# Optimization experiments

Hardware: AMD Instinct MI355X
Metric: run time of the kernel (lower is better)

## Reference

```python
import jax, jax.numpy as jnp
import numpy as np

N = 8192
IN_F = 512
OUT_F = 512
N_SUB = 8


def setup_inputs() -> dict:
    key = jax.random.key(0)
    k1, k2, k3, k4 = jax.random.split(key, 4)
    input_features = jax.random.normal(k1, (N, IN_F), dtype=jnp.float32)
    # dense adjacency with small positive entries (normalized-adj-like)
    adj = jax.random.uniform(k2, (N, N), dtype=jnp.float32) / N
    subspace_labels = jax.random.randint(k3, (N,), 0, N_SUB, dtype=jnp.int32)
    # kaiming-uniform-style init per subspace weight
    bound = float(np.sqrt(6.0 / IN_F))
    W = jax.random.uniform(k4, (N_SUB, IN_F, OUT_F), dtype=jnp.float32,
                           minval=-bound, maxval=bound)
    return {"input_features": input_features, "adj": adj,
            "subspace_labels": subspace_labels, "W": W}


def reference(input_features, adj, subspace_labels, W):
    # Original: for each subspace s,
    #   output[mask_s] = adj[mask_s][:, mask_s] @ (X[mask_s] @ W[s])
    # Equivalently: per-node support uses that node's subspace weight, and
    # adjacency is masked to same-subspace pairs.
    n_sub = W.shape[0]
    support = jnp.zeros((input_features.shape[0], W.shape[2]),
                        dtype=input_features.dtype)
    for s in range(n_sub):  # small fixed loop over subspaces
        sel = (subspace_labels == s)[:, None]
        support = support + jnp.where(sel, input_features @ W[s], 0.0)
    # mask adjacency to intra-subspace edges: [N, N]
    same = (subspace_labels[:, None] == subspace_labels[None, :])
    masked_adj = jnp.where(same, adj, 0.0)
    return masked_adj @ support
```

## Files before the change

kernel.cpp:

```cpp
#include <hip/hip_runtime.h>
#include <hip/hip_bf16.h>

#define NN   8192
#define FF   512
#define NS   8
#define CAP  1152
#define KKT  (NS * CAP)

typedef __bf16 bf16x8 __attribute__((ext_vector_type(8)));
typedef float  f32x4  __attribute__((ext_vector_type(4)));

__global__ void bucket_kernel(const int* __restrict__ labels,
                              int* __restrict__ permP,
                              int* __restrict__ kk_of) {
    __shared__ int off8[NS];
    int t = threadIdx.x;
    if (t < NS) off8[t] = 0;
    for (int i = t; i < KKT; i += 256) permP[i] = -1;
    __syncthreads();
    for (int i = t; i < NN; i += 256) {
        int s = labels[i];
        int p = atomicAdd(&off8[s], 1);
        if (p < CAP) {
            int pos = s * CAP + p;
            permP[pos] = i;
            kk_of[i] = pos;
        } else {
            kk_of[i] = -1;
        }
    }
}

__global__ void wt_kernel(const float* __restrict__ W, __bf16* __restrict__ WT) {
    __shared__ float tile[32][33];
    int s  = blockIdx.z;
    int n0 = blockIdx.x * 32, k0 = blockIdx.y * 32;
    int tx = threadIdx.x, ty = threadIdx.y;
    const float* Ws = W + (size_t)s * FF * FF;
    for (int r = 0; r < 4; ++r) {
        int k = k0 + ty + r * 8;
        tile[ty + r * 8][tx] = Ws[(size_t)k * FF + n0 + tx];
    }
    __syncthreads();
    __bf16* WTs = WT + (size_t)s * FF * FF;
    for (int r = 0; r < 4; ++r) {
        int n = n0 + ty + r * 8;
        WTs[(size_t)n * FF + k0 + tx] = (__bf16)tile[tx][ty + r * 8];
    }
}

__global__ __launch_bounds__(512) void support_kernel(
        const float* __restrict__ X, const __bf16* __restrict__ WT,
        const int* __restrict__ permP, __bf16* __restrict__ supT) {
    __shared__ __align__(16) __bf16 Alds[4][32][8];
    __shared__ __align__(16) __bf16 Blds[4][512][8];
    __shared__ int nodes[32];
    const int t = threadIdx.x, lane = t & 63, w = t >> 6;
    const int ii0 = blockIdx.x * 32;
    const int seg = ii0 / CAP;
    const int mh = w & 1, nq = w >> 1, l15 = lane & 15, q = lane >> 4;
    f32x4 acc[8] = {};
    if (t < 32) nodes[t] = permP[ii0 + t];
    __syncthreads();
    const __bf16* Wseg = WT + (size_t)seg * FF * FF;
    for (int k0 = 0; k0 < FF; k0 += 32) {
        #pragma unroll
        for (int pass = 0; pass < 4; ++pass) {
            int slot = pass * 512 + t;
            int c = slot & 3, n = slot >> 2;
            uint4 tmp = *(const uint4*)(Wseg + (size_t)n * FF + k0 + c * 8);
            *(uint4*)&Blds[c][n][0] = tmp;
        }
        if (t < 256) {
            int m = t >> 3, c = t & 7;
            int node = nodes[m];
            __align__(8) __bf16 v[4];
            if (node >= 0) {
                float4 xv = *(const float4*)(X + (size_t)node * FF + k0 + c * 4);
                v[0] = (__bf16)xv.x; v[1] = (__bf16)xv.y;
                v[2] = (__bf16)xv.z; v[3] = (__bf16)xv.w;
            } else {
                v[0] = v[1] = v[2] = v[3] = (__bf16)0.0f;
            }
            int kq = c >> 1, off = (c & 1) * 4;
            *(uint2*)&Alds[kq][m][off] = *(uint2*)v;
        }
        __syncthreads();
        bf16x8 af = *(bf16x8*)&Alds[q][mh * 16 + l15][0];
        int nbase = nq * 128 + l15;
        #pragma unroll
        for (int nt = 0; nt < 8; ++nt) {
            bf16x8 bfr = *(bf16x8*)&Blds[q][nbase + nt * 16][0];
            acc[nt] = __builtin_amdgcn_mfma_f32_16x16x32_bf16(af, bfr, acc[nt], 0, 0, 0);
        }
        __syncthreads();
    }
    int kkb = ii0 + mh * 16 + q * 4;
    #pragma unroll
    for (int nt = 0; nt < 8; ++nt) {
        int n = nq * 128 + nt * 16 + l15;
        __align__(8) __bf16 v[4];
        #pragma unroll
        for (int r = 0; r < 4; ++r) v[r] = (__bf16)acc[nt][r];
        *(uint2*)(supT + (size_t)n * KKT + kkb) = *(uint2*)v;
    }
}

__global__ __launch_bounds__(256) void compact_kernel(
        const float* __restrict__ adj, const int* __restrict__ permP,
        const int* __restrict__ kk_of, __bf16* __restrict__ adjc) {
    int ii = blockIdx.x;
    int node = permP[ii];
    if (node < 0) return;
    int base = (ii / CAP) * CAP;
    __bf16* dst = adjc + (size_t)ii * CAP;
    const float4* arow = (const float4*)(adj + (size_t)node * NN);
    const int4*  kkrow = (const int4*)kk_of;
    int t = threadIdx.x;
    #pragma unroll
    for (int p = 0; p < NN / (256 * 4); ++p) {
        int idx = p * 256 + t;
        float4 a = arow[idx];
        int4  kk = kkrow[idx];
        int j;
        j = kk.x - base; if ((unsigned)j < CAP) dst[j] = (__bf16)a.x;
        j = kk.y - base; if ((unsigned)j < CAP) dst[j] = (__bf16)a.y;
        j = kk.z - base; if ((unsigned)j < CAP) dst[j] = (__bf16)a.z;
        j = kk.w - base; if ((unsigned)j < CAP) dst[j] = (__bf16)a.w;
    }
}

__global__ __launch_bounds__(512) void gemm_kernel(
        const __bf16* __restrict__ adjc, const __bf16* __restrict__ supT,
        const int* __restrict__ permP, float* __restrict__ out) {
    __shared__ __align__(16) __bf16 Alds[4][32][8];
    __shared__ __align__(16) __bf16 Blds[4][512][8];
    const int t = threadIdx.x, lane = t & 63, w = t >> 6;
    const int ii0 = blockIdx.x * 32;
    const int seg = ii0 / CAP, base = seg * CAP;
    const int mh = w & 1, nq = w >> 1, l15 = lane & 15, q = lane >> 4;
    f32x4 acc[8] = {};
    const __bf16* Ag = adjc + (size_t)ii0 * CAP;
    for (int j0 = 0; j0 < CAP; j0 += 32) {
        #pragma unroll
        for (int pass = 0; pass < 4; ++pass) {
            int slot = pass * 512 + t;
            int c = slot & 3, n = slot >> 2;
            uint4 tmp = *(const uint4*)(supT + (size_t)n * KKT + base + j0 + c * 8);
            *(uint4*)&Blds[c][n][0] = tmp;
        }
        if (t < 128) {
            int m = t >> 2, c = t & 3;
            uint4 tmp = *(const uint4*)(Ag + (size_t)m * CAP + j0 + c * 8);
            *(uint4*)&Alds[c][m][0] = tmp;
        }
        __syncthreads();
        bf16x8 af = *(bf16x8*)&Alds[q][mh * 16 + l15][0];
        int nbase = nq * 128 + l15;
        #pragma unroll
        for (int nt = 0; nt < 8; ++nt) {
            bf16x8 bfr = *(bf16x8*)&Blds[q][nbase + nt * 16][0];
            acc[nt] = __builtin_amdgcn_mfma_f32_16x16x32_bf16(af, bfr, acc[nt], 0, 0, 0);
        }
        __syncthreads();
    }
    int rowb = ii0 + mh * 16 + q * 4;
    #pragma unroll
    for (int r = 0; r < 4; ++r) {
        int node = permP[rowb + r];
        if (node >= 0) {
            float* o = out + (size_t)node * FF + nq * 128 + l15;
            #pragma unroll
            for (int nt = 0; nt < 8; ++nt) o[nt * 16] = acc[nt][r];
        }
    }
}

extern "C" void kernel_launch(void* const* d_in, const int* in_sizes, int n_in,
                              void* d_out, int out_size, void* d_ws, size_t ws_size,
                              hipStream_t stream) {
    const float* X      = (const float*)d_in[0];
    const float* adj    = (const float*)d_in[1];
    const int*   labels = (const int*)d_in[2];
    const float* W      = (const float*)d_in[3];
    float* out = (float*)d_out;

    char* ws = (char*)d_ws;
    int*    kk_of = (int*)(ws + 1024);
    int*    permP = (int*)(ws + (64u << 10));
    __bf16* WT    = (__bf16*)(ws + (1u << 20));
    __bf16* supT  = (__bf16*)(ws + (6u << 20));
    __bf16* adjc  = (__bf16*)(ws + (16u << 20));

    hipMemsetAsync(adjc, 0, (size_t)KKT * CAP * sizeof(__bf16), stream);
    bucket_kernel<<<1, 256, 0, stream>>>(labels, permP, kk_of);
    wt_kernel<<<dim3(16, 16, 8), dim3(32, 8), 0, stream>>>(W, WT);
    support_kernel<<<KKT / 32, 512, 0, stream>>>(X, WT, permP, supT);
    compact_kernel<<<KKT, 256, 0, stream>>>(adj, permP, kk_of, adjc);
    gemm_kernel<<<KKT / 32, 512, 0, stream>>>(adjc, supT, permP, out);
}
```

Before: 513.5 us.

## Use direct global-to-LDS loads, parallel bucketing, LDS-staged compaction, block swizzle

Replaces register-staged tile loads in the support and adjacency GEMMs with global_load_lds, which writes straight into shared memory. Bucketing now runs across many blocks using global atomics instead of a single block. Compaction builds each row in LDS and writes it out densely, which removes the large memset of the compacted adjacency. Block indices are swizzled so that concurrently running blocks cover different segments. Atomic bucketing makes node order nondeterministic, and the new LDS layout has to match what the MFMA fragment reads expect.

```diff
diff --git a/kernel.cpp b/kernel.cpp
--- a/kernel.cpp
+++ b/kernel.cpp
@@ -10,24 +10,24 @@
 typedef __bf16 bf16x8 __attribute__((ext_vector_type(8)));
 typedef float  f32x4  __attribute__((ext_vector_type(4)));
 
+#define GLOAD_LDS(src, dst)                                                    \
+    __builtin_amdgcn_global_load_lds(                                          \
+        (const __attribute__((address_space(1))) void*)(src),                  \
+        (__attribute__((address_space(3))) void*)(dst), 16, 0, 0)
+
 __global__ void bucket_kernel(const int* __restrict__ labels,
                               int* __restrict__ permP,
-                              int* __restrict__ kk_of) {
-    __shared__ int off8[NS];
-    int t = threadIdx.x;
-    if (t < NS) off8[t] = 0;
-    for (int i = t; i < KKT; i += 256) permP[i] = -1;
-    __syncthreads();
-    for (int i = t; i < NN; i += 256) {
-        int s = labels[i];
-        int p = atomicAdd(&off8[s], 1);
-        if (p < CAP) {
-            int pos = s * CAP + p;
-            permP[pos] = i;
-            kk_of[i] = pos;
-        } else {
-            kk_of[i] = -1;
-        }
+                              int* __restrict__ kk_of,
+                              int* __restrict__ cnt) {
+    int i = blockIdx.x * 256 + threadIdx.x;
+    int s = labels[i];
+    int p = atomicAdd(&cnt[s], 1);
+    if (p < CAP) {
+        int pos = s * CAP + p;
+        permP[pos] = i;
+        kk_of[i] = pos;
+    } else {
+        kk_of[i] = -1;
     }
 }
 
@@ -56,7 +56,8 @@
     __shared__ __align__(16) __bf16 Blds[4][512][8];
     __shared__ int nodes[32];
     const int t = threadIdx.x, lane = t & 63, w = t >> 6;
-    const int ii0 = blockIdx.x * 32;
+    const int bswz = (blockIdx.x & 7) * 36 + (blockIdx.x >> 3);
+    const int ii0 = bswz * 32;
     const int seg = ii0 / CAP;
     const int mh = w & 1, nq = w >> 1, l15 = lane & 15, q = lane >> 4;
     f32x4 acc[8] = {};
@@ -66,10 +67,8 @@
     for (int k0 = 0; k0 < FF; k0 += 32) {
         #pragma unroll
         for (int pass = 0; pass < 4; ++pass) {
-            int slot = pass * 512 + t;
-            int c = slot & 3, n = slot >> 2;
-            uint4 tmp = *(const uint4*)(Wseg + (size_t)n * FF + k0 + c * 8);
-            *(uint4*)&Blds[c][n][0] = tmp;
+            const __bf16* src = Wseg + (size_t)t * FF + k0 + pass * 8;
+            GLOAD_LDS(src, &Blds[pass][w * 64][0]);
         }
         if (t < 256) {
             int m = t >> 3, c = t & 7;
@@ -109,24 +108,32 @@
 __global__ __launch_bounds__(256) void compact_kernel(
         const float* __restrict__ adj, const int* __restrict__ permP,
         const int* __restrict__ kk_of, __bf16* __restrict__ adjc) {
+    __shared__ __align__(16) __bf16 row[CAP];
+    int t = threadIdx.x;
     int ii = blockIdx.x;
+    #pragma unroll
+    for (int i = t; i < CAP * 2 / 4; i += 256) ((int*)row)[i] = 0;
     int node = permP[ii];
-    if (node < 0) return;
-    int base = (ii / CAP) * CAP;
-    __bf16* dst = adjc + (size_t)ii * CAP;
-    const float4* arow = (const float4*)(adj + (size_t)node * NN);
-    const int4*  kkrow = (const int4*)kk_of;
-    int t = threadIdx.x;
-    #pragma unroll
-    for (int p = 0; p < NN / (256 * 4); ++p) {
-        int idx = p * 256 + t;
-        float4 a = arow[idx];
-        int4  kk = kkrow[idx];
-        int j;
-        j = kk.x - base; if ((unsigned)j < CAP) dst[j] = (__bf16)a.x;
-        j = kk.y - base; if ((unsigned)j < CAP) dst[j] = (__bf16)a.y;
-        j = kk.z - base; if ((unsigned)j < CAP) dst[j] = (__bf16)a.z;
-        j = kk.w - base; if ((unsigned)j < CAP) dst[j] = (__bf16)a.w;
+    __syncthreads();
+    if (node >= 0) {
+        int base = (ii / CAP) * CAP;
+        const float4* arow = (const float4*)(adj + (size_t)node * NN);
+        const int4*  kkrow = (const int4*)kk_of;
+        #pragma unroll
+        for (int p = 0; p < NN / (256 * 4); ++p) {
+            int idx = p * 256 + t;
+            float4 a = arow[idx];
+            int4  kk = kkrow[idx];
+            int j;
+            j = kk.x - base; if ((unsigned)j < CAP) row[j] = (__bf16)a.x;
+            j = kk.y - base; if ((unsigned)j < CAP) row[j] = (__bf16)a.y;
+            j = kk.z - base; if ((unsigned)j < CAP) row[j] = (__bf16)a.z;
+            j = kk.w - base; if ((unsigned)j < CAP) row[j] = (__bf16)a.w;
+        }
+    }
+    __syncthreads();
+    if (t < CAP * 2 / 16) {
+        ((uint4*)(adjc + (size_t)ii * CAP))[t] = ((const uint4*)row)[t];
     }
 }
 
@@ -136,7 +143,8 @@
     __shared__ __align__(16) __bf16 Alds[4][32][8];
     __shared__ __align__(16) __bf16 Blds[4][512][8];
     const int t = threadIdx.x, lane = t & 63, w = t >> 6;
-    const int ii0 = blockIdx.x * 32;
+    const int bswz = (blockIdx.x & 7) * 36 + (blockIdx.x >> 3);
+    const int ii0 = bswz * 32;
     const int seg = ii0 / CAP, base = seg * CAP;
     const int mh = w & 1, nq = w >> 1, l15 = lane & 15, q = lane >> 4;
     f32x4 acc[8] = {};
@@ -144,15 +152,12 @@
     for (int j0 = 0; j0 < CAP; j0 += 32) {
         #pragma unroll
         for (int pass = 0; pass < 4; ++pass) {
-            int slot = pass * 512 + t;
-            int c = slot & 3, n = slot >> 2;
-            uint4 tmp = *(const uint4*)(supT + (size_t)n * KKT + base + j0 + c * 8);
-            *(uint4*)&Blds[c][n][0] = tmp;
+            const __bf16* src = supT + (size_t)t * KKT + base + j0 + pass * 8;
+            GLOAD_LDS(src, &Blds[pass][w * 64][0]);
         }
         if (t < 128) {
-            int m = t >> 2, c = t & 3;
-            uint4 tmp = *(const uint4*)(Ag + (size_t)m * CAP + j0 + c * 8);
-            *(uint4*)&Alds[c][m][0] = tmp;
+            const __bf16* srcA = Ag + (size_t)(t & 31) * CAP + j0 + (t >> 5) * 8;
+            GLOAD_LDS(srcA, &Alds[0][0][0] + (size_t)(w * 64) * 8);
         }
         __syncthreads();
         bf16x8 af = *(bf16x8*)&Alds[q][mh * 16 + l15][0];
@@ -186,14 +191,16 @@
     float* out = (float*)d_out;
 
     char* ws = (char*)d_ws;
+    int*    cnt   = (int*)ws;
     int*    kk_of = (int*)(ws + 1024);
     int*    permP = (int*)(ws + (64u << 10));
     __bf16* WT    = (__bf16*)(ws + (1u << 20));
     __bf16* supT  = (__bf16*)(ws + (6u << 20));
     __bf16* adjc  = (__bf16*)(ws + (16u << 20));
 
-    hipMemsetAsync(adjc, 0, (size_t)KKT * CAP * sizeof(__bf16), stream);
-    bucket_kernel<<<1, 256, 0, stream>>>(labels, permP, kk_of);
+    hipMemsetAsync(cnt, 0, NS * sizeof(int), stream);
+    hipMemsetAsync(permP, 0xFF, (size_t)KKT * sizeof(int), stream);
+    bucket_kernel<<<NN / 256, 256, 0, stream>>>(labels, permP, kk_of, cnt);
     wt_kernel<<<dim3(16, 16, 8), dim3(32, 8), 0, stream>>>(W, WT);
     support_kernel<<<KKT / 32, 512, 0, stream>>>(X, WT, permP, supT);
     compact_kernel<<<KKT, 256, 0, stream>>>(adj, permP, kk_of, adjc);
```

After: 587.1 us. 14.3% more time.
